# Kernel optimization log

Measured on AMD Instinct MI355X. Metric: run time of the kernel, lower is better.

## Reference

```python
import jax, jax.numpy as jnp
import numpy as np

N_DYADIC = 0  # dyadic refinement order 'n' from SigLoss_MMD.__init__


def _sig_gram(X, Y, n):
    """Gram matrix of signature kernels k(x_i, y_j) via the first-order
    finite-difference PDE scheme used by sig_kernels_f/fb_mmd:
        K[i+1,j+1] = K[i+1,j] + K[i,j+1] + K[i,j]*(<dx_i, dy_j> - 1)
    with dyadically refined increments dx = (x_{t+1}-x_t)/2^n repeated 2^n times.
    X: (A, M, D), Y: (B, N, D) -> returns (A, B) = K[:, :, -1, -1].
    The row recurrence is a cumulative sum, so each PDE row is one cumsum
    (fully vectorized over all (A,B) pairs); lax.scan runs over rows.
    """
    f = 2 ** n
    incX = jnp.repeat((X[:, 1:] - X[:, :-1]) / f, f, axis=1)  # (A, MM, D)
    incY = jnp.repeat((Y[:, 1:] - Y[:, :-1]) / f, f, axis=1)  # (B, NN, D)
    Mmat = jnp.einsum('aid,bjd->abij', incX, incY)            # (A, B, MM, NN)
    A, B, MM, NN = Mmat.shape
    ones_col = jnp.ones((A, B, 1), Mmat.dtype)
    row0 = jnp.ones((A, B, NN + 1), Mmat.dtype)               # K[0, :] = 1

    def step(prev_row, Mrow):  # prev_row: (A,B,NN+1), Mrow: (A,B,NN)
        # K[i+1,j+1] - K[i+1,j] = K[i,j+1] + K[i,j]*(M[i,j]-1)  -> cumsum
        inc = prev_row[..., 1:] + prev_row[..., :-1] * (Mrow - 1.0)
        new_row = jnp.concatenate([ones_col, 1.0 + jnp.cumsum(inc, axis=-1)], axis=-1)
        return new_row, None

    last_row, _ = jax.lax.scan(step, row0, jnp.moveaxis(Mmat, 2, 0))
    return last_row[..., -1]  # (A, B)


def setup_inputs() -> dict:
    key = jax.random.key(0)
    kx, ky = jax.random.split(key)
    A, M, D = 64, 128, 128
    SCALE = 0.025  # keeps increment inner products small so the PDE stays bounded
    X = SCALE * jax.random.normal(kx, (A, M, D), dtype=jnp.float32)
    Y = SCALE * jax.random.normal(ky, (A, M, D), dtype=jnp.float32)
    return {"X": X, "Y": Y}


def reference(X, Y):
    K_XX = _sig_gram(X, X, N_DYADIC)
    K_YY = _sig_gram(Y, Y, N_DYADIC)
    K_XY = _sig_gram(X, Y, N_DYADIC)
    mmd_squared = jnp.mean(K_XX) + jnp.mean(K_YY) - 2.0 * jnp.mean(K_XY)
    return mmd_squared
```

## Files before the change

### kernel.cpp

```cpp
#include <hip/hip_runtime.h>
#include <hip/hip_bf16.h>

#define MM 127
#define CHUNK_U16 4096
#define MAT_U16   16384
#define ARR_U16   1048576
#define QS_STRIDE 136
#define QS_DWORDS (64 * QS_STRIDE)

typedef __attribute__((ext_vector_type(8))) short short8;
typedef __attribute__((ext_vector_type(4))) float floatx4;

__device__ __forceinline__ unsigned int pack_bf16_rne(float a, float b) {
  float2 rr; rr.x = a; rr.y = b;
  __hip_bfloat162 hp = __float22bfloat162_rn(rr);
  unsigned int hu; __builtin_memcpy(&hu, &hp, 4);
  return hu;
}

__device__ __forceinline__ float wave_shr1(float x) {
  return __int_as_float(__builtin_amdgcn_update_dpp(
      0, __float_as_int(x), 0x138, 0xf, 0xf, true));
}

__global__ __launch_bounds__(256) void prep_kernel(
    const float* __restrict__ X, const float* __restrict__ Y,
    unsigned short* __restrict__ base, float* __restrict__ acc)
{
  if (blockIdx.x == 0 && threadIdx.x == 0) acc[0] = 0.f;
  const int bid = blockIdx.x;
  const int c = bid & 3;
  const int m = (bid >> 2) & 63;
  const int isY = bid >> 8;
  const float* src = (isY ? Y : X) + m * 128 * 128;
  unsigned short* dst = base + isY * ARR_U16 + m * MAT_U16 + c * CHUNK_U16;

  for (int s = threadIdx.x; s < 512; s += 256) {
    const int r = s >> 2;
    const int g = (s & 3) ^ ((r >> 1) & 3);
    uint4 hv = make_uint4(0, 0, 0, 0);
    if (r < MM) {
      const float* p = src + r * 128 + c * 32 + g * 8;
      float4 u0 = *reinterpret_cast<const float4*>(p);
      float4 u1 = *reinterpret_cast<const float4*>(p + 4);
      float4 v0 = *reinterpret_cast<const float4*>(p + 128);
      float4 v1 = *reinterpret_cast<const float4*>(p + 132);
      hv.x = pack_bf16_rne(v0.x - u0.x, v0.y - u0.y);
      hv.y = pack_bf16_rne(v0.z - u0.z, v0.w - u0.w);
      hv.z = pack_bf16_rne(v1.x - u1.x, v1.y - u1.y);
      hv.w = pack_bf16_rne(v1.z - u1.z, v1.w - u1.w);
    }
    *reinterpret_cast<uint4*>(dst + s * 8) = hv;
  }
}

__global__ __launch_bounds__(256, 1) void sig_pair_kernel(
    const unsigned short* __restrict__ base, float* __restrict__ acc)
{
  __shared__ unsigned int smw[4 * QS_DWORDS];
  const int tid = threadIdx.x;
  const int wid = tid >> 6, lane = tid & 63;
  const int p0 = blockIdx.x * 4 + wid;

  float w;
  int a, b, srcA, srcB;
  if (p0 < 4160) {
    int p = p0;
    srcA = 0;
    if (p >= 2080) { p -= 2080; srcA = 1; }
    srcB = srcA;
    int ia = (int)((sqrtf(8.0f * (float)p + 1.0f) - 1.0f) * 0.5f);
    while ((ia + 1) * (ia + 2) / 2 <= p) ia++;
    while (ia * (ia + 1) / 2 > p) ia--;
    int ib = p - ia * (ia + 1) / 2;
    a = ia; b = ib;
    w = (a == b ? 1.0f : 2.0f) / 4096.0f;
  } else {
    int p = p0 - 4160;
    a = p >> 6; b = p & 63;
    srcA = 0; srcB = 1;
    w = -2.0f / 4096.0f;
  }
  const unsigned short* Am = base + srcA * ARR_U16 + a * MAT_U16;
  const unsigned short* Bm = base + srcB * ARR_U16 + b * MAT_U16;

  unsigned int* const myw = smw + wid * QS_DWORDS;
  unsigned short* const mys = reinterpret_cast<unsigned short*>(myw);
  const int lrow = lane & 15, quad = lane >> 4;

  {
    uint4 z = make_uint4(0u, 0u, 0u, 0u);
    uint4* w4 = reinterpret_cast<uint4*>(myw);
    for (int i = lane; i < QS_DWORDS / 4; i += 64) w4[i] = z;
  }

  short8 bh[8][4];
#pragma unroll
  for (int tc = 0; tc < 8; ++tc) {
    const int r = tc * 16 + lrow;
    const int ro = r * 32 + ((quad ^ ((r >> 1) & 3)) * 8);
#pragma unroll
    for (int c = 0; c < 4; ++c)
      bh[tc][c] = *reinterpret_cast<const short8*>(&Bm[c * CHUNK_U16 + ro]);
  }

#pragma unroll 1
  for (int tr = 0; tr < 8; ++tr) {
    const int r = tr * 16 + lrow;
    const int ro = r * 32 + ((quad ^ ((r >> 1) & 3)) * 8);
    short8 ah[4];
#pragma unroll
    for (int c = 0; c < 4; ++c)
      ah[c] = *reinterpret_cast<const short8*>(&Am[c * CHUNK_U16 + ro]);

    const int im0 = tr * 16 + quad * 4;
#pragma unroll
    for (int tc = 0; tc < 8; ++tc) {
      floatx4 a4 = (floatx4){0.f, 0.f, 0.f, 0.f};
#pragma unroll
      for (int c = 0; c < 4; ++c)
        a4 = __builtin_amdgcn_mfma_f32_16x16x32_bf16(ah[c], bh[tc][c], a4, 0, 0, 0);
      const int jm = tc * 16 + lrow;
      if (jm < MM) {
        const int lt = (jm + 1) >> 1;
        const int half = (jm & 1) ? 0 : 1;
        const int phys0 = im0 + jm + 5 - 4 * (lt >> 1) - 4 * (lt & 1);
        unsigned short* pp = &mys[(lt * QS_STRIDE + phys0) * 2 + half];
        unsigned int u01 = pack_bf16_rne(a4[0], a4[1]);
        unsigned int u23 = pack_bf16_rne(a4[2], a4[3]);
        pp[0] = (unsigned short)u01;
        pp[2] = (unsigned short)(u01 >> 16);
        pp[4] = (unsigned short)u23;
        if (im0 + 3 < MM) pp[6] = (unsigned short)(u23 >> 16);
      }
    }
  }

  {
    const int l = lane;
    const int shift = 4 * (l >> 1) + 4 * (l & 1) - 4;
    const unsigned int lbase = l * QS_STRIDE;

    auto loadg = [&](int g) -> uint4 {
      int pb = 4 * g - shift;
      pb = pb < 0 ? 132 : (pb > 128 ? 128 : pb);
      return *reinterpret_cast<const uint4*>(&myw[lbase + pb]);
    };

    float curE = 1.f, curO = 1.f;
    float npE = (l == 0) ? 0.f : 1.f, npO = 1.f;
    uint4 P0 = loadg(0), P1 = loadg(1);

    for (int g = 0; g < 63; ++g) {
      const uint4 cur = P0;
      P0 = P1;
      if (g < 62) P1 = loadg(g + 2);
      unsigned int uu[4] = {cur.x, cur.y, cur.z, cur.w};
#pragma unroll
      for (int e = 0; e < 4; ++e) {
        unsigned int u = uu[e];
        float mE = __uint_as_float(u << 16) - 1.0f;
        float mO = __uint_as_float(u & 0xFFFF0000u) - 1.0f;
        float ncE = wave_shr1(curO);
        float ncO = curE;
        float vE = (curE + npE * mE) + ncE;
        float vO = (curO + npO * mO) + ncO;
        npE = ncE; npO = ncO;
        curE = vE; curO = vO;
      }
    }
    {
      unsigned int uu[2] = {P0.x, P0.y};
#pragma unroll
      for (int e = 0; e < 2; ++e) {
        unsigned int u = uu[e];
        float mE = __uint_as_float(u << 16) - 1.0f;
        float mO = __uint_as_float(u & 0xFFFF0000u) - 1.0f;
        float ncE = wave_shr1(curO);
        float ncO = curE;
        float vE = (curE + npE * mE) + ncE;
        float vO = (curO + npO * mO) + ncO;
        npE = ncE; npO = ncO;
        curE = vE; curO = vO;
      }
    }
    if (l == 63) atomicAdd(acc, w * curO);
  }
}

__global__ void finalize_kernel(const float* __restrict__ acc,
                                unsigned int* __restrict__ out) {
  float v = acc[0];
  __hip_bfloat16 bv = __float2bfloat16(v);
  unsigned short u;
  __builtin_memcpy(&u, &bv, sizeof(u));
  out[0] = ((unsigned int)u << 16) | (unsigned int)u;
}

extern "C" void kernel_launch(void* const* d_in, const int* in_sizes, int n_in,
                              void* d_out, int out_size, void* d_ws, size_t ws_size,
                              hipStream_t stream) {
  const float* X = (const float*)d_in[0];
  const float* Y = (const float*)d_in[1];
  float* acc = (float*)d_ws;
  unsigned short* base = (unsigned short*)((char*)d_ws + 1024);

  prep_kernel<<<512, 256, 0, stream>>>(X, Y, base, acc);
  sig_pair_kernel<<<2064, 256, 0, stream>>>(base, acc);
  finalize_kernel<<<1, 1, 0, stream>>>(acc, (unsigned int*)d_out);
}
```

Measured before the change: 210.3 us.

## Split each pair across producer and consumer waves with anti-diagonal pipelining

Each block now handles one (a,b) pair instead of four. Three producer waves compute the 16x16 MFMA tiles of the increment Gram matrix along anti-diagonals into shared memory, while one consumer wave runs the PDE wavefront recurrence on the diagonals already written, with a barrier after each diagonal. The aim is to overlap the serial recurrence with the matrix products and to raise occupancy through smaller LDS use and launch_bounds(256,4). In exchange, 15 block barriers are added, B tiles are reloaded from global memory per tile instead of being held in registers, and four times as many blocks are launched.

Result: slower. 269.5 us (+28.1%).

```diff
diff --git a/kernel.cpp b/kernel.cpp
--- a/kernel.cpp
+++ b/kernel.cpp
@@ -54,18 +54,18 @@
   }
 }
 
-__global__ __launch_bounds__(256, 1) void sig_pair_kernel(
+__global__ __launch_bounds__(256, 4) void sig_pair_kernel(
     const unsigned short* __restrict__ base, float* __restrict__ acc)
 {
-  __shared__ unsigned int smw[4 * QS_DWORDS];
+  __shared__ unsigned int smw[QS_DWORDS];
+  unsigned short* const sm = reinterpret_cast<unsigned short*>(smw);
   const int tid = threadIdx.x;
-  const int wid = tid >> 6, lane = tid & 63;
-  const int p0 = blockIdx.x * 4 + wid;
+  const int bid = blockIdx.x;
 
   float w;
   int a, b, srcA, srcB;
-  if (p0 < 4160) {
-    int p = p0;
+  if (bid < 4160) {
+    int p = bid;
     srcA = 0;
     if (p >= 2080) { p -= 2080; srcA = 1; }
     srcB = srcA;
@@ -76,7 +76,7 @@
     a = ia; b = ib;
     w = (a == b ? 1.0f : 2.0f) / 4096.0f;
   } else {
-    int p = p0 - 4160;
+    int p = bid - 4160;
     a = p >> 6; b = p & 63;
     srcA = 0; srcB = 1;
     w = -2.0f / 4096.0f;
@@ -84,107 +84,94 @@
   const unsigned short* Am = base + srcA * ARR_U16 + a * MAT_U16;
   const unsigned short* Bm = base + srcB * ARR_U16 + b * MAT_U16;
 
-  unsigned int* const myw = smw + wid * QS_DWORDS;
-  unsigned short* const mys = reinterpret_cast<unsigned short*>(myw);
+  const int wid = tid >> 6, lane = tid & 63;
   const int lrow = lane & 15, quad = lane >> 4;
 
   {
     uint4 z = make_uint4(0u, 0u, 0u, 0u);
-    uint4* w4 = reinterpret_cast<uint4*>(myw);
-    for (int i = lane; i < QS_DWORDS / 4; i += 64) w4[i] = z;
+    uint4* smw4 = reinterpret_cast<uint4*>(smw);
+    for (int i = tid; i < QS_DWORDS / 4; i += 256) smw4[i] = z;
   }
+  __syncthreads();
 
-  short8 bh[8][4];
+  const int cw = (bid >> 8) & 3;
+  const bool isCons = (wid == cw);
+  const int p = (wid < cw) ? wid : wid - 1;
+
+  const int shift = 4 * (lane >> 1) + 4 * (lane & 1) - 4;
+  const unsigned int lbase = lane * QS_STRIDE;
+  float curE = 1.f, curO = 1.f;
+  float npE = (lane == 0) ? 0.f : 1.f, npO = 1.f;
+
+  auto loadg = [&](int g) -> uint4 {
+    int pb = 4 * g - shift;
+    pb = pb < 0 ? 132 : (pb > 128 ? 128 : pb);
+    return *reinterpret_cast<const uint4*>(&smw[lbase + pb]);
+  };
+  auto estep = [&](unsigned int u) {
+    float mE = __uint_as_float(u << 16) - 1.0f;
+    float mO = __uint_as_float(u & 0xFFFF0000u) - 1.0f;
+    float ncE = wave_shr1(curO);
+    float ncO = curE;
+    float vE = (curE + npE * mE) + ncE;
+    float vO = (curO + npO * mO) + ncO;
+    npE = ncE; npO = ncO;
+    curE = vE; curO = vO;
+  };
+  auto do4 = [&](uint4 cur) {
+    estep(cur.x); estep(cur.y); estep(cur.z); estep(cur.w);
+  };
+
+  for (int d = 0; d < 15; ++d) {
+    if (!isCons) {
+      const int tlo = (d > 7) ? (d - 7) : 0;
+      const int thi = (d < 7) ? d : 7;
+      int k = 0;
+      for (int tr = tlo; tr <= thi; ++tr, ++k) {
+        if ((k % 3) != p) continue;
+        const int tc = d - tr;
+        const int ra = tr * 16 + lrow;
+        const int oa = ra * 32 + ((quad ^ ((ra >> 1) & 3)) * 8);
+        const int rb = tc * 16 + lrow;
+        const int ob = rb * 32 + ((quad ^ ((rb >> 1) & 3)) * 8);
+        floatx4 a4 = (floatx4){0.f, 0.f, 0.f, 0.f};
 #pragma unroll
-  for (int tc = 0; tc < 8; ++tc) {
-    const int r = tc * 16 + lrow;
-    const int ro = r * 32 + ((quad ^ ((r >> 1) & 3)) * 8);
-#pragma unroll
-    for (int c = 0; c < 4; ++c)
-      bh[tc][c] = *reinterpret_cast<const short8*>(&Bm[c * CHUNK_U16 + ro]);
-  }
-
-#pragma unroll 1
-  for (int tr = 0; tr < 8; ++tr) {
-    const int r = tr * 16 + lrow;
-    const int ro = r * 32 + ((quad ^ ((r >> 1) & 3)) * 8);
-    short8 ah[4];
-#pragma unroll
-    for (int c = 0; c < 4; ++c)
-      ah[c] = *reinterpret_cast<const short8*>(&Am[c * CHUNK_U16 + ro]);
-
-    const int im0 = tr * 16 + quad * 4;
-#pragma unroll
-    for (int tc = 0; tc < 8; ++tc) {
-      floatx4 a4 = (floatx4){0.f, 0.f, 0.f, 0.f};
-#pragma unroll
-      for (int c = 0; c < 4; ++c)
-        a4 = __builtin_amdgcn_mfma_f32_16x16x32_bf16(ah[c], bh[tc][c], a4, 0, 0, 0);
-      const int jm = tc * 16 + lrow;
-      if (jm < MM) {
-        const int lt = (jm + 1) >> 1;
-        const int half = (jm & 1) ? 0 : 1;
-        const int phys0 = im0 + jm + 5 - 4 * (lt >> 1) - 4 * (lt & 1);
-        unsigned short* pp = &mys[(lt * QS_STRIDE + phys0) * 2 + half];
-        unsigned int u01 = pack_bf16_rne(a4[0], a4[1]);
-        unsigned int u23 = pack_bf16_rne(a4[2], a4[3]);
-        pp[0] = (unsigned short)u01;
-        pp[2] = (unsigned short)(u01 >> 16);
-        pp[4] = (unsigned short)u23;
-        if (im0 + 3 < MM) pp[6] = (unsigned short)(u23 >> 16);
+        for (int c = 0; c < 4; ++c) {
+          short8 ah = *reinterpret_cast<const short8*>(&Am[c * CHUNK_U16 + oa]);
+          short8 bh = *reinterpret_cast<const short8*>(&Bm[c * CHUNK_U16 + ob]);
+          a4 = __builtin_amdgcn_mfma_f32_16x16x32_bf16(ah, bh, a4, 0, 0, 0);
+        }
+        const int jm = tc * 16 + lrow;
+        if (jm < MM) {
+          const int im0 = tr * 16 + quad * 4;
+          const int lt = (jm + 1) >> 1;
+          const int half = (jm & 1) ? 0 : 1;
+          const int phys0 = im0 + jm + 5 - 4 * (lt >> 1) - 4 * (lt & 1);
+          unsigned short* pp = &sm[(lt * QS_STRIDE + phys0) * 2 + half];
+          unsigned int u01 = pack_bf16_rne(a4[0], a4[1]);
+          unsigned int u23 = pack_bf16_rne(a4[2], a4[3]);
+          pp[0] = (unsigned short)u01;
+          pp[2] = (unsigned short)(u01 >> 16);
+          pp[4] = (unsigned short)u23;
+          if (im0 + 3 < MM) pp[6] = (unsigned short)(u23 >> 16);
+        }
       }
+      asm volatile("s_waitcnt lgkmcnt(0)" ::: "memory");
+    }
+    __builtin_amdgcn_s_barrier();
+    asm volatile("" ::: "memory");
+    if (isCons) {
+      const int g0 = 4 * d;
+      uint4 Q0 = loadg(g0),     Q1 = loadg(g0 + 1);
+      uint4 Q2 = loadg(g0 + 2), Q3 = loadg(g0 + 3);
+      do4(Q0); do4(Q1); do4(Q2); do4(Q3);
     }
   }
-
-  {
-    const int l = lane;
-    const int shift = 4 * (l >> 1) + 4 * (l & 1) - 4;
-    const unsigned int lbase = l * QS_STRIDE;
-
-    auto loadg = [&](int g) -> uint4 {
-      int pb = 4 * g - shift;
-      pb = pb < 0 ? 132 : (pb > 128 ? 128 : pb);
-      return *reinterpret_cast<const uint4*>(&myw[lbase + pb]);
-    };
-
-    float curE = 1.f, curO = 1.f;
-    float npE = (l == 0) ? 0.f : 1.f, npO = 1.f;
-    uint4 P0 = loadg(0), P1 = loadg(1);
-
-    for (int g = 0; g < 63; ++g) {
-      const uint4 cur = P0;
-      P0 = P1;
-      if (g < 62) P1 = loadg(g + 2);
-      unsigned int uu[4] = {cur.x, cur.y, cur.z, cur.w};
-#pragma unroll
-      for (int e = 0; e < 4; ++e) {
-        unsigned int u = uu[e];
-        float mE = __uint_as_float(u << 16) - 1.0f;
-        float mO = __uint_as_float(u & 0xFFFF0000u) - 1.0f;
-        float ncE = wave_shr1(curO);
-        float ncO = curE;
-        float vE = (curE + npE * mE) + ncE;
-        float vO = (curO + npO * mO) + ncO;
-        npE = ncE; npO = ncO;
-        curE = vE; curO = vO;
-      }
-    }
-    {
-      unsigned int uu[2] = {P0.x, P0.y};
-#pragma unroll
-      for (int e = 0; e < 2; ++e) {
-        unsigned int u = uu[e];
-        float mE = __uint_as_float(u << 16) - 1.0f;
-        float mO = __uint_as_float(u & 0xFFFF0000u) - 1.0f;
-        float ncE = wave_shr1(curO);
-        float ncO = curE;
-        float vE = (curE + npE * mE) + ncE;
-        float vO = (curO + npO * mO) + ncO;
-        npE = ncE; npO = ncO;
-        curE = vE; curO = vO;
-      }
-    }
-    if (l == 63) atomicAdd(acc, w * curO);
+  if (isCons) {
+    uint4 Q0 = loadg(60), Q1 = loadg(61), Q2 = loadg(62), Q3 = loadg(63);
+    do4(Q0); do4(Q1); do4(Q2);
+    estep(Q3.x); estep(Q3.y);
+    if (lane == 63) atomicAdd(acc, w * curO);
   }
 }
 
@@ -206,6 +193,6 @@
   unsigned short* base = (unsigned short*)((char*)d_ws + 1024);
 
   prep_kernel<<<512, 256, 0, stream>>>(X, Y, base, acc);
-  sig_pair_kernel<<<2064, 256, 0, stream>>>(base, acc);
+  sig_pair_kernel<<<8256, 256, 0, stream>>>(base, acc);
   finalize_kernel<<<1, 1, 0, stream>>>(acc, (unsigned int*)d_out);
 }
```
